# Performance work log

Hardware: AMD Instinct MI355X
Metric: run time of the kernel (lower is better)

The kernel has to match this reference:

```python
import jax, jax.numpy as jnp
import numpy as np
from jax import lax

B, S, P, H = 256, 336, 96, 512


def setup_inputs() -> dict:
    key = jax.random.key(0)
    ks = jax.random.split(key, 18)
    def n(k, shape, s=0.05):
        return jax.random.normal(k, shape, dtype=jnp.float32) * s
    return {
        "x": jax.random.normal(ks[0], (B, S, 7), dtype=jnp.float32),
        "lin_enc_w": n(ks[1], (H, 3)), "lin_enc_b": n(ks[2], (H,)),
        "quat_enc_w": n(ks[3], (H, 4)), "quat_enc_b": n(ks[4], (H,)),
        "lin_wih": n(ks[5], (4 * H, H)), "lin_whh": n(ks[6], (4 * H, H)),
        "lin_bih": n(ks[7], (4 * H,)), "lin_bhh": n(ks[8], (4 * H,)),
        "quat_wih": n(ks[9], (4 * H, H)), "quat_whh": n(ks[10], (4 * H, H)),
        "quat_bih": n(ks[11], (4 * H,)), "quat_bhh": n(ks[12], (4 * H,)),
        "lin_dec_w": n(ks[13], (3, H)), "lin_dec_b": n(ks[14], (3,)),
        "quat_dec_w": n(ks[15], (4, H)), "quat_dec_b": n(ks[16], (4,)),
        "pred_len": P,
    }


def _lstm_cell(carry, xt, Wih, Whh, bih, bhh):
    # PyTorch gate order: i, f, g, o
    h, c = carry
    g = xt @ Wih.T + bih + h @ Whh.T + bhh  # [B, 4H]
    i, f, gg, o = jnp.split(g, 4, axis=-1)
    c = jax.nn.sigmoid(f) * c + jax.nn.sigmoid(i) * jnp.tanh(gg)
    h = jax.nn.sigmoid(o) * jnp.tanh(c)
    return (h, c), h


def _branch(xc, We, be, Wih, Whh, bih, bhh, Wd, bd, pred_len):
    e = xc @ We.T + be  # [B, S, H]
    Bn, _, Hn = e.shape
    cell = lambda carry, xt: _lstm_cell(carry, xt, Wih, Whh, bih, bhh)
    z = jnp.zeros((Bn, Hn), e.dtype)
    (h, _), outs = lax.scan(cell, (z, z), jnp.swapaxes(e, 0, 1))  # outs: [S, B, H]
    # Each prediction step feeds h as input to the LSTM with ZERO initial state
    # (the original code does not pass (h, c) back in).
    def pred_step(h, _):
        (hn, _), _ = cell((jnp.zeros_like(h), jnp.zeros_like(h)), h)
        return hn, hn
    _, preds = lax.scan(pred_step, h, None, length=pred_len)  # [P, B, H]
    seq = jnp.concatenate([outs, preds], axis=0)[1:]  # drop first step -> [S+P-1, B, H]
    return jnp.swapaxes(seq, 0, 1) @ Wd.T + bd


def reference(x, lin_enc_w, lin_enc_b, quat_enc_w, quat_enc_b,
              lin_wih, lin_whh, lin_bih, lin_bhh,
              quat_wih, quat_whh, quat_bih, quat_bhh,
              lin_dec_w, lin_dec_b, quat_dec_w, quat_dec_b, pred_len):
    lx = _branch(x[:, :, :3], lin_enc_w, lin_enc_b, lin_wih, lin_whh,
                 lin_bih, lin_bhh, lin_dec_w, lin_dec_b, pred_len)
    rx = _branch(x[:, :, 3:], quat_enc_w, quat_enc_b, quat_wih, quat_whh,
                 quat_bih, quat_bhh, quat_dec_w, quat_dec_b, pred_len)
    return jnp.concatenate([lx, rx], axis=2)  # [B, S+P-1, 7]
```

## Files before the change

### kernel.cpp

```cpp
#include <hip/hip_runtime.h>

#define BB 256
#define SS 336
#define HH 512
#define NT 431
#define NU 432

typedef __attribute__((ext_vector_type(8))) short bf16x8;
typedef __attribute__((ext_vector_type(16))) float f32x16;
typedef __attribute__((ext_vector_type(4))) int i32x4;


__device__ inline unsigned short f2bf(float f) {
    unsigned int u = __float_as_uint(f);
    unsigned int r = (u + 0x7fffu + ((u >> 16) & 1u)) >> 16;
    return (unsigned short)r;
}
__device__ inline float sigm(float x) { return 1.f / (1.f + __expf(-x)); }
__device__ inline float tanh_(float x) { return 2.f / (1.f + __expf(-2.f * x)) - 1.f; }

__device__ inline i32x4 llc_load_b128(const i32x4* p) {
    i32x4 r;
    asm volatile("global_load_dwordx4 %0, %1, off sc0 sc1" : "=v"(r) : "v"(p));
    return r;
}
__device__ inline void llc_store_b128(i32x4* p, i32x4 v) {
    asm volatile("global_store_dwordx4 %0, %1, off sc0 sc1" :: "v"(p), "v"(v) : "memory");
}
__device__ inline void vm_drain() { asm volatile("s_waitcnt vmcnt(0)" ::: "memory"); }

__global__ void k_wfrag(const float* __restrict__ w0, const float* __restrict__ w1,
                        const float* __restrict__ w2, const float* __restrict__ w3,
                        unsigned short* __restrict__ wfrag) {
    int idx = blockIdx.x * 256 + threadIdx.x;
    int mat = idx >> 17;
    int t = idx & 131071;
    int lane = t & 63;
    int kb = (t >> 6) & 31;
    int wq = (t >> 11) & 3;
    int cg = t >> 13;
    const float* W = mat == 0 ? w0 : (mat == 1 ? w1 : (mat == 2 ? w2 : w3));
    int n = wq * 512 + cg * 32 + (lane & 31);
    int k0 = kb * 16 + (lane >> 5) * 8;
    const float* src = W + n * 512 + k0;
    unsigned short us[8];
#pragma unroll
    for (int j = 0; j < 8; ++j) us[j] = f2bf(src[j]);
    i32x4 v;
    v.x = us[0] | (us[1] << 16); v.y = us[2] | (us[3] << 16);
    v.z = us[4] | (us[5] << 16); v.w = us[6] | (us[7] << 16);
    ((i32x4*)wfrag)[idx] = v;
}

__global__ void k_mbias(const float* __restrict__ lin_wih, const float* __restrict__ quat_wih,
                        const float* __restrict__ lin_enc_w, const float* __restrict__ quat_enc_w,
                        const float* __restrict__ lin_enc_b, const float* __restrict__ quat_enc_b,
                        const float* __restrict__ lin_bih, const float* __restrict__ lin_bhh,
                        const float* __restrict__ quat_bih, const float* __restrict__ quat_bhh,
                        float* __restrict__ M, float* __restrict__ bE, float* __restrict__ bP) {
    int gid = blockIdx.x * 256 + threadIdx.x;
    int branch = gid >> 11;
    int n = gid & 2047;
    int nf = 3 + branch;
    const float* Wih = branch ? quat_wih : lin_wih;
    const float* We  = branch ? quat_enc_w : lin_enc_w;
    const float* be  = branch ? quat_enc_b : lin_enc_b;
    const float* bih = branch ? quat_bih : lin_bih;
    const float* bhh = branch ? quat_bhh : lin_bhh;
    float m[4] = {0.f, 0.f, 0.f, 0.f};
    float bs = 0.f;
    for (int j = 0; j < 512; ++j) {
        float w = Wih[n * 512 + j];
#pragma unroll
        for (int kf = 0; kf < 4; ++kf)
            if (kf < nf) m[kf] += w * We[j * nf + kf];
        bs += w * be[j];
    }
    float* Mp = M + (branch * 2048 + n) * 4;
#pragma unroll
    for (int kf = 0; kf < 4; ++kf) Mp[kf] = m[kf];
    bE[branch * 2048 + n] = bs + bih[n] + bhh[n];
    bP[branch * 2048 + n] = bih[n] + bhh[n];
}

__global__ void k_zero(i32x4* __restrict__ p) {
    int idx = blockIdx.x * 256 + threadIdx.x;
    p[idx] = i32x4{0, 0, 0, 0};
}

__global__ __launch_bounds__(256, 1) void k_persist(
    const float* __restrict__ x,
    const unsigned short* __restrict__ wfrag,
    const float* __restrict__ M, const float* __restrict__ bE, const float* __restrict__ bP,
    const float* __restrict__ lin_dec_w, const float* __restrict__ quat_dec_w,
    const float* __restrict__ lin_dec_b, const float* __restrict__ quat_dec_b,
    unsigned short* __restrict__ hbuf,
    float* __restrict__ out,
    unsigned int* __restrict__ bar) {
    __shared__ i32x4 lds_a[2][2048];
    __shared__ float g_lds[32 * 132];
    __shared__ float h_tile[32 * 33];
    __shared__ float mE[512];
    __shared__ float bEs[128];
    __shared__ float bPs[128];

    const int tid = threadIdx.x;
    const int lane = tid & 63;
    const int wv = tid >> 6;
    const int blk = blockIdx.x;
    const int branch = blk >> 7;
    const int rg = (blk >> 4) & 7;
    const int cg = blk & 15;
    const int group = blk >> 4;
    const int nf = 3 + branch;
    const int row = tid & 31;
    const int jbase = tid >> 5;
    const int b = rg * 32 + row;

    for (int t = tid; t < 512; t += 256) {
        int gate = t >> 7, jj = (t >> 2) & 31, kf = t & 3;
        mE[t] = M[(size_t)(branch * 2048 + gate * 512 + cg * 32 + jj) * 4 + kf];
    }
    if (tid < 128) {
        int gate = tid >> 5, jj = tid & 31;
        bEs[tid] = bE[branch * 2048 + gate * 512 + cg * 32 + jj];
        bPs[tid] = bP[branch * 2048 + gate * 512 + cg * 32 + jj];
    }

    const int dr   = lane & 1;
    const int dd   = (lane >> 1) & 3;
    const int dseg = lane >> 3;
    const int drow = cg * 2 + dr;
    const bool dvalid = dd < nf;
    const float* dwp = (branch ? quat_dec_w : lin_dec_w) + dd * 512;
    const float dbias = dvalid ? (branch ? quat_dec_b : lin_dec_b)[dd] : 0.f;

    const i32x4* BpE = (const i32x4*)wfrag + (size_t)(branch * 2) * 131072
                       + ((cg * 4 + wv) * 32) * 64 + lane;
    const i32x4* BpP = BpE + 131072;
    i32x4 bw[32];
#pragma unroll
    for (int kb = 0; kb < 32; ++kb) bw[kb] = BpE[kb * 64];

    float creg[4] = {0.f, 0.f, 0.f, 0.f};
    unsigned int* myslot = bar + (size_t)blk * 16;

    __syncthreads();

    for (int u = 0; u <= NU; ++u) {
        const int is_enc = (u < SS);

        float xv0 = 0.f, xv1 = 0.f, xv2 = 0.f, xv3 = 0.f;
        if (is_enc) {
            const float* xp = x + ((size_t)b * SS + u) * 7 + branch * 3;
            xv0 = xp[0]; xv1 = xp[1]; xv2 = xp[2];
            if (branch) xv3 = xp[3];
        }
        if (u == SS) {
#pragma unroll
            for (int kb = 0; kb < 32; ++kb) bw[kb] = BpP[kb * 64];
        }

        if (u > 0) {
            if (wv == 0) {
                const unsigned int* slot = bar + (size_t)((group << 4) | (lane & 15)) * 16;
                for (;;) {
                    unsigned int v;
                    asm volatile("global_load_dword %0, %1, off sc0 sc1\n\ts_waitcnt vmcnt(0)"
                                 : "=v"(v) : "v"(slot) : "memory");
                    if (__all((int)(v >= (unsigned int)u))) break;
                    __builtin_amdgcn_s_sleep(1);
                }
            }
            __syncthreads();
        }

        i32x4* lds_cur = lds_a[u & 1];
        {
            const i32x4* gsrc = (const i32x4*)hbuf + (size_t)(u & 1) * 32768
                                + (size_t)branch * 16384 + rg * 2048 + tid;
            i32x4 av[8];
#pragma unroll
            for (int i = 0; i < 8; ++i) av[i] = llc_load_b128(gsrc + i * 256);
            vm_drain();
            __builtin_amdgcn_sched_barrier(0);
#pragma unroll
            for (int i = 0; i < 8; ++i) lds_cur[i * 256 + tid] = av[i];
        }
        __syncthreads();

        if (u == NU) {
            if (wv == 3) {
                float s = 0.f;
                if (dvalid) {
                    const unsigned short* hp = (const unsigned short*)lds_cur;
#pragma unroll
                    for (int jj = 0; jj < 64; ++jj) {
                        int j = dseg * 64 + jj;
                        unsigned short hu = hp[(j >> 4) * 512 + ((j >> 3) & 1) * 256 + drow * 8 + (j & 7)];
                        s += __uint_as_float(((unsigned int)hu) << 16) * dwp[j];
                    }
                }
                s += __shfl_xor(s, 8);
                s += __shfl_xor(s, 16);
                s += __shfl_xor(s, 32);
                if (dseg == 0 && dvalid)
                    out[((size_t)(rg * 32 + drow) * NT + (u - 2)) * 7 + branch * 3 + dd] = s + dbias;
            }
            break;
        }

        f32x16 acc = {};
        const i32x4* Afrag = lds_cur + lane;
#pragma unroll
        for (int kb = 0; kb < 32; ++kb) {
            i32x4 a0 = Afrag[kb * 64];
            acc = __builtin_amdgcn_mfma_f32_32x32x16_bf16(*(const bf16x8*)&a0, *(const bf16x8*)&bw[kb], acc, 0, 0, 0);
        }
        {
            int col_l = wv * 32 + (lane & 31);
            int rbase = 4 * (lane >> 5);
#pragma unroll
            for (int r = 0; r < 16; ++r) {
                int row_l = rbase + (r & 3) + 8 * (r >> 2);
                g_lds[row_l * 132 + col_l] = acc[r];
            }
        }
        __syncthreads();

#pragma unroll
        for (int p = 0; p < 4; ++p) {
            int jj = jbase * 4 + p;
            float gi = g_lds[row * 132 + jj];
            float gf = g_lds[row * 132 + 32 + jj];
            float gc = g_lds[row * 132 + 64 + jj];
            float go = g_lds[row * 132 + 96 + jj];
            if (is_enc) {
                int j4 = jj * 4;
                gi += bEs[jj]      + xv0 * mE[j4]       + xv1 * mE[j4 + 1]       + xv2 * mE[j4 + 2]       + xv3 * mE[j4 + 3];
                gf += bEs[32 + jj] + xv0 * mE[128 + j4] + xv1 * mE[128 + j4 + 1] + xv2 * mE[128 + j4 + 2] + xv3 * mE[128 + j4 + 3];
                gc += bEs[64 + jj] + xv0 * mE[256 + j4] + xv1 * mE[256 + j4 + 1] + xv2 * mE[256 + j4 + 2] + xv3 * mE[256 + j4 + 3];
                go += bEs[96 + jj] + xv0 * mE[384 + j4] + xv1 * mE[384 + j4 + 1] + xv2 * mE[384 + j4 + 2] + xv3 * mE[384 + j4 + 3];
            } else {
                gi += bPs[jj];
                gf += bPs[32 + jj];
                gc += bPs[64 + jj];
                go += bPs[96 + jj];
            }
            float iv = sigm(gi), fv = sigm(gf), gv = tanh_(gc), ov = sigm(go);
            float cn;
            if (is_enc) {
                cn = fv * creg[p] + iv * gv;
                creg[p] = cn;
            } else {
                cn = iv * gv;
            }
            h_tile[row * 33 + jj] = ov * tanh_(cn);
        }
        __syncthreads();

        if (wv == 0) {
#pragma unroll
            for (int chunk = 0; chunk < 2; ++chunk) {
                int row_l = lane & 31;
                int ch = chunk * 16 + (lane >> 5) * 8;
                unsigned short us[8];
#pragma unroll
                for (int j = 0; j < 8; ++j) us[j] = f2bf(h_tile[row_l * 33 + ch + j]);
                i32x4 v;
                v.x = us[0] | (us[1] << 16); v.y = us[2] | (us[3] << 16);
                v.z = us[4] | (us[5] << 16); v.w = us[6] | (us[7] << 16);
                int kb = cg * 2 + chunk;
                llc_store_b128((i32x4*)hbuf + (size_t)((u + 1) & 1) * 32768
                               + (size_t)branch * 16384 + rg * 2048 + kb * 64 + lane, v);
            }
            vm_drain();
            if (lane == 0) {
                unsigned int fl = (unsigned int)(u + 1);
                asm volatile("global_store_dword %0, %1, off sc0 sc1" :: "v"(myslot), "v"(fl) : "memory");
            }
        } else if (wv == 3 && u >= 2) {
            float s = 0.f;
            if (dvalid) {
                const unsigned short* hp = (const unsigned short*)lds_cur;
#pragma unroll
                for (int jj = 0; jj < 64; ++jj) {
                    int j = dseg * 64 + jj;
                    unsigned short hu = hp[(j >> 4) * 512 + ((j >> 3) & 1) * 256 + drow * 8 + (j & 7)];
                    s += __uint_as_float(((unsigned int)hu) << 16) * dwp[j];
                }
            }
            s += __shfl_xor(s, 8);
            s += __shfl_xor(s, 16);
            s += __shfl_xor(s, 32);
            if (dseg == 0 && dvalid)
                out[((size_t)(rg * 32 + drow) * NT + (u - 2)) * 7 + branch * 3 + dd] = s + dbias;
        }
    }
}

extern "C" void kernel_launch(void* const* d_in, const int* in_sizes, int n_in,
                              void* d_out, int out_size, void* d_ws, size_t ws_size,
                              hipStream_t stream) {
    const float* x          = (const float*)d_in[0];
    const float* lin_enc_w  = (const float*)d_in[1];
    const float* lin_enc_b  = (const float*)d_in[2];
    const float* quat_enc_w = (const float*)d_in[3];
    const float* quat_enc_b = (const float*)d_in[4];
    const float* lin_wih    = (const float*)d_in[5];
    const float* lin_whh    = (const float*)d_in[6];
    const float* lin_bih    = (const float*)d_in[7];
    const float* lin_bhh    = (const float*)d_in[8];
    const float* quat_wih   = (const float*)d_in[9];
    const float* quat_whh   = (const float*)d_in[10];
    const float* quat_bih   = (const float*)d_in[11];
    const float* quat_bhh   = (const float*)d_in[12];
    const float* lin_dec_w  = (const float*)d_in[13];
    const float* lin_dec_b  = (const float*)d_in[14];
    const float* quat_dec_w = (const float*)d_in[15];
    const float* quat_dec_b = (const float*)d_in[16];
    float* out = (float*)d_out;
    char* ws = (char*)d_ws;

    unsigned short* wfrag = (unsigned short*)(ws + 0);
    unsigned short* hbuf  = (unsigned short*)(ws + 8388608ull);
    unsigned int*   bar   = (unsigned int*)(ws + 9437184ull);
    float* M    = (float*)(ws + 10485760ull);
    float* bE   = (float*)(ws + 10551296ull);
    float* bP   = (float*)(ws + 10567680ull);

    k_wfrag<<<2048, 256, 0, stream>>>(lin_whh, lin_wih, quat_whh, quat_wih, wfrag);
    k_mbias<<<16, 256, 0, stream>>>(lin_wih, quat_wih, lin_enc_w, quat_enc_w,
                                    lin_enc_b, quat_enc_b, lin_bih, lin_bhh,
                                    quat_bih, quat_bhh, M, bE, bP);
    k_zero<<<260, 256, 0, stream>>>((i32x4*)(ws + 8388608ull));

    k_persist<<<256, 256, 0, stream>>>(x, wfrag, M, bE, bP, lin_dec_w, quat_dec_w,
                                       lin_dec_b, quat_dec_b, hbuf, out, bar);
}
```

Measured before the change: 2.997 ms.

## Interleave two batch cohorts per persistent block to hide inter-block barrier latency

```diff
diff --git a/kernel.cpp b/kernel.cpp
--- a/kernel.cpp
+++ b/kernel.cpp
@@ -98,7 +98,7 @@
     float* __restrict__ out,
     unsigned int* __restrict__ bar) {
     __shared__ i32x4 lds_a[2][2048];
-    __shared__ float g_lds[32 * 132];
+    __shared__ float g_lds[32 * 133];
     __shared__ float h_tile[32 * 33];
     __shared__ float mE[512];
     __shared__ float bEs[128];
@@ -108,15 +108,12 @@
     const int lane = tid & 63;
     const int wv = tid >> 6;
     const int blk = blockIdx.x;
-    const int branch = blk >> 7;
-    const int rg = (blk >> 4) & 7;
+    const int branch = blk >> 6;
+    const int rgl = (blk >> 4) & 3;
     const int cg = blk & 15;
-    const int group = blk >> 4;
     const int nf = 3 + branch;
     const int row = tid & 31;
     const int jbase = tid >> 5;
-    const int b = rg * 32 + row;
-
     for (int t = tid; t < 512; t += 256) {
         int gate = t >> 7, jj = (t >> 2) & 31, kf = t & 3;
         mE[t] = M[(size_t)(branch * 2048 + gate * 512 + cg * 32 + jj) * 4 + kf];
@@ -142,55 +139,154 @@
 #pragma unroll
     for (int kb = 0; kb < 32; ++kb) bw[kb] = BpE[kb * 64];
 
-    float creg[4] = {0.f, 0.f, 0.f, 0.f};
-    unsigned int* myslot = bar + (size_t)blk * 16;
+    float creg[2][4] = {{0.f, 0.f, 0.f, 0.f}, {0.f, 0.f, 0.f, 0.f}};
 
     __syncthreads();
 
     for (int u = 0; u <= NU; ++u) {
         const int is_enc = (u < SS);
-
-        float xv0 = 0.f, xv1 = 0.f, xv2 = 0.f, xv3 = 0.f;
-        if (is_enc) {
-            const float* xp = x + ((size_t)b * SS + u) * 7 + branch * 3;
-            xv0 = xp[0]; xv1 = xp[1]; xv2 = xp[2];
-            if (branch) xv3 = xp[3];
-        }
         if (u == SS) {
 #pragma unroll
             for (int kb = 0; kb < 32; ++kb) bw[kb] = BpP[kb * 64];
         }
 
-        if (u > 0) {
+#pragma unroll
+        for (int coh = 0; coh < 2; ++coh) {
+            const int rgt = coh * 4 + rgl;
+            const int b = coh * 128 + rgl * 32 + row;
+
+            float xv0 = 0.f, xv1 = 0.f, xv2 = 0.f, xv3 = 0.f;
+            if (is_enc) {
+                const float* xp = x + ((size_t)b * SS + u) * 7 + branch * 3;
+                xv0 = xp[0]; xv1 = xp[1]; xv2 = xp[2];
+                if (branch) xv3 = xp[3];
+            }
+
+            if (u > 0) {
+                if (wv == 0) {
+                    const unsigned int* slot = bar
+                        + (size_t)((((branch << 3) | (coh << 2) | rgl) << 4) | (lane & 15)) * 16;
+                    int guard = 0;
+                    for (;;) {
+                        unsigned int v = 0xFFFFFFFFu;
+                        if (lane < 16)
+                            asm volatile("global_load_dword %0, %1, off sc0 sc1\n\ts_waitcnt vmcnt(0)"
+                                         : "=v"(v) : "v"(slot) : "memory");
+                        if (__all((int)(v >= (unsigned int)u))) break;
+                        if (++guard > (1 << 18)) break;
+                        __builtin_amdgcn_s_sleep(1);
+                    }
+                }
+                __syncthreads();
+            }
+
+            i32x4* lds_cur = lds_a[coh];
+            {
+                const i32x4* gsrc = (const i32x4*)hbuf + (size_t)(u & 1) * 32768
+                                    + (size_t)branch * 16384 + rgt * 2048 + tid;
+                i32x4 av[8];
+#pragma unroll
+                for (int i = 0; i < 8; ++i) av[i] = llc_load_b128(gsrc + i * 256);
+                vm_drain();
+                __builtin_amdgcn_sched_barrier(0);
+#pragma unroll
+                for (int i = 0; i < 8; ++i) lds_cur[i * 256 + tid] = av[i];
+            }
+            __syncthreads();
+
+            if (u == NU) {
+                if (wv == 3) {
+                    float s = 0.f;
+                    if (dvalid) {
+                        const unsigned short* hp = (const unsigned short*)lds_cur;
+#pragma unroll
+                        for (int jj = 0; jj < 64; ++jj) {
+                            int j = dseg * 64 + jj;
+                            unsigned short hu = hp[(j >> 4) * 512 + ((j >> 3) & 1) * 256 + drow * 8 + (j & 7)];
+                            s += __uint_as_float(((unsigned int)hu) << 16) * dwp[j];
+                        }
+                    }
+                    s += __shfl_xor(s, 8);
+                    s += __shfl_xor(s, 16);
+                    s += __shfl_xor(s, 32);
+                    if (dseg == 0 && dvalid)
+                        out[((size_t)(coh * 128 + rgl * 32 + drow) * NT + (u - 2)) * 7 + branch * 3 + dd] = s + dbias;
+                }
+                continue;
+            }
+
+            f32x16 acc = {};
+            const i32x4* Afrag = lds_cur + lane;
+#pragma unroll
+            for (int kb = 0; kb < 32; ++kb) {
+                i32x4 a0 = Afrag[kb * 64];
+                acc = __builtin_amdgcn_mfma_f32_32x32x16_bf16(*(const bf16x8*)&a0, *(const bf16x8*)&bw[kb], acc, 0, 0, 0);
+            }
+            {
+                int col_l = wv * 32 + (lane & 31);
+                int rbase = 4 * (lane >> 5);
+#pragma unroll
+                for (int r = 0; r < 16; ++r) {
+                    int row_l = rbase + (r & 3) + 8 * (r >> 2);
+                    g_lds[row_l * 133 + col_l] = acc[r];
+                }
+            }
+            __syncthreads();
+
+#pragma unroll
+            for (int p = 0; p < 4; ++p) {
+                int jj = jbase * 4 + p;
+                float gi = g_lds[row * 133 + jj];
+                float gf = g_lds[row * 133 + 32 + jj];
+                float gc = g_lds[row * 133 + 64 + jj];
+                float go = g_lds[row * 133 + 96 + jj];
+                if (is_enc) {
+                    int j4 = jj * 4;
+                    gi += bEs[jj]      + xv0 * mE[j4]       + xv1 * mE[j4 + 1]       + xv2 * mE[j4 + 2]       + xv3 * mE[j4 + 3];
+                    gf += bEs[32 + jj] + xv0 * mE[128 + j4] + xv1 * mE[128 + j4 + 1] + xv2 * mE[128 + j4 + 2] + xv3 * mE[128 + j4 + 3];
+                    gc += bEs[64 + jj] + xv0 * mE[256 + j4] + xv1 * mE[256 + j4 + 1] + xv2 * mE[256 + j4 + 2] + xv3 * mE[256 + j4 + 3];
+                    go += bEs[96 + jj] + xv0 * mE[384 + j4] + xv1 * mE[384 + j4 + 1] + xv2 * mE[384 + j4 + 2] + xv3 * mE[384 + j4 + 3];
+                } else {
+                    gi += bPs[jj];
+                    gf += bPs[32 + jj];
+                    gc += bPs[64 + jj];
+                    go += bPs[96 + jj];
+                }
+                float iv = sigm(gi), fv = sigm(gf), gv = tanh_(gc), ov = sigm(go);
+                float cn;
+                if (is_enc) {
+                    cn = fv * creg[coh][p] + iv * gv;
+                    creg[coh][p] = cn;
+                } else {
+                    cn = iv * gv;
+                }
+                h_tile[row * 33 + jj] = ov * tanh_(cn);
+            }
+            __syncthreads();
+
             if (wv == 0) {
-                const unsigned int* slot = bar + (size_t)((group << 4) | (lane & 15)) * 16;
-                for (;;) {
-                    unsigned int v;
-                    asm volatile("global_load_dword %0, %1, off sc0 sc1\n\ts_waitcnt vmcnt(0)"
-                                 : "=v"(v) : "v"(slot) : "memory");
-                    if (__all((int)(v >= (unsigned int)u))) break;
-                    __builtin_amdgcn_s_sleep(1);
-                }
-            }
-            __syncthreads();
-        }
-
-        i32x4* lds_cur = lds_a[u & 1];
-        {
-            const i32x4* gsrc = (const i32x4*)hbuf + (size_t)(u & 1) * 32768
-                                + (size_t)branch * 16384 + rg * 2048 + tid;
-            i32x4 av[8];
-#pragma unroll
-            for (int i = 0; i < 8; ++i) av[i] = llc_load_b128(gsrc + i * 256);
-            vm_drain();
-            __builtin_amdgcn_sched_barrier(0);
-#pragma unroll
-            for (int i = 0; i < 8; ++i) lds_cur[i * 256 + tid] = av[i];
-        }
-        __syncthreads();
-
-        if (u == NU) {
-            if (wv == 3) {
+#pragma unroll
+                for (int chunk = 0; chunk < 2; ++chunk) {
+                    int row_l = lane & 31;
+                    int ch = chunk * 16 + (lane >> 5) * 8;
+                    unsigned short us[8];
+#pragma unroll
+                    for (int j = 0; j < 8; ++j) us[j] = f2bf(h_tile[row_l * 33 + ch + j]);
+                    i32x4 v;
+                    v.x = us[0] | (us[1] << 16); v.y = us[2] | (us[3] << 16);
+                    v.z = us[4] | (us[5] << 16); v.w = us[6] | (us[7] << 16);
+                    int kb = cg * 2 + chunk;
+                    llc_store_b128((i32x4*)hbuf + (size_t)((u + 1) & 1) * 32768
+                                   + (size_t)branch * 16384 + rgt * 2048 + kb * 64 + lane, v);
+                }
+                vm_drain();
+                if (lane == 0) {
+                    unsigned int fl = (unsigned int)(u + 1);
+                    unsigned int* myslot = bar
+                        + (size_t)((((branch << 3) | (coh << 2) | rgl) << 4) | cg) * 16;
+                    asm volatile("global_store_dword %0, %1, off sc0 sc1" :: "v"(myslot), "v"(fl) : "memory");
+                }
+            } else if (wv == 3 && u >= 2) {
                 float s = 0.f;
                 if (dvalid) {
                     const unsigned short* hp = (const unsigned short*)lds_cur;
@@ -205,97 +301,11 @@
                 s += __shfl_xor(s, 16);
                 s += __shfl_xor(s, 32);
                 if (dseg == 0 && dvalid)
-                    out[((size_t)(rg * 32 + drow) * NT + (u - 2)) * 7 + branch * 3 + dd] = s + dbias;
-            }
-            break;
+                    out[((size_t)(coh * 128 + rgl * 32 + drow) * NT + (u - 2)) * 7 + branch * 3 + dd] = s + dbias;
+            }
         }
 
-        f32x16 acc = {};
-        const i32x4* Afrag = lds_cur + lane;
-#pragma unroll
-        for (int kb = 0; kb < 32; ++kb) {
-            i32x4 a0 = Afrag[kb * 64];
-            acc = __builtin_amdgcn_mfma_f32_32x32x16_bf16(*(const bf16x8*)&a0, *(const bf16x8*)&bw[kb], acc, 0, 0, 0);
-        }
-        {
-            int col_l = wv * 32 + (lane & 31);
-            int rbase = 4 * (lane >> 5);
-#pragma unroll
-            for (int r = 0; r < 16; ++r) {
-                int row_l = rbase + (r & 3) + 8 * (r >> 2);
-                g_lds[row_l * 132 + col_l] = acc[r];
-            }
-        }
-        __syncthreads();
-
-#pragma unroll
-        for (int p = 0; p < 4; ++p) {
-            int jj = jbase * 4 + p;
-            float gi = g_lds[row * 132 + jj];
-            float gf = g_lds[row * 132 + 32 + jj];
-            float gc = g_lds[row * 132 + 64 + jj];
-            float go = g_lds[row * 132 + 96 + jj];
-            if (is_enc) {
-                int j4 = jj * 4;
-                gi += bEs[jj]      + xv0 * mE[j4]       + xv1 * mE[j4 + 1]       + xv2 * mE[j4 + 2]       + xv3 * mE[j4 + 3];
-                gf += bEs[32 + jj] + xv0 * mE[128 + j4] + xv1 * mE[128 + j4 + 1] + xv2 * mE[128 + j4 + 2] + xv3 * mE[128 + j4 + 3];
-                gc += bEs[64 + jj] + xv0 * mE[256 + j4] + xv1 * mE[256 + j4 + 1] + xv2 * mE[256 + j4 + 2] + xv3 * mE[256 + j4 + 3];
-                go += bEs[96 + jj] + xv0 * mE[384 + j4] + xv1 * mE[384 + j4 + 1] + xv2 * mE[384 + j4 + 2] + xv3 * mE[384 + j4 + 3];
-            } else {
-                gi += bPs[jj];
-                gf += bPs[32 + jj];
-                gc += bPs[64 + jj];
-                go += bPs[96 + jj];
-            }
-            float iv = sigm(gi), fv = sigm(gf), gv = tanh_(gc), ov = sigm(go);
-            float cn;
-            if (is_enc) {
-                cn = fv * creg[p] + iv * gv;
-                creg[p] = cn;
-            } else {
-                cn = iv * gv;
-            }
-            h_tile[row * 33 + jj] = ov * tanh_(cn);
-        }
-        __syncthreads();
-
-        if (wv == 0) {
-#pragma unroll
-            for (int chunk = 0; chunk < 2; ++chunk) {
-                int row_l = lane & 31;
-                int ch = chunk * 16 + (lane >> 5) * 8;
-                unsigned short us[8];
-#pragma unroll
-                for (int j = 0; j < 8; ++j) us[j] = f2bf(h_tile[row_l * 33 + ch + j]);
-                i32x4 v;
-                v.x = us[0] | (us[1] << 16); v.y = us[2] | (us[3] << 16);
-                v.z = us[4] | (us[5] << 16); v.w = us[6] | (us[7] << 16);
-                int kb = cg * 2 + chunk;
-                llc_store_b128((i32x4*)hbuf + (size_t)((u + 1) & 1) * 32768
-                               + (size_t)branch * 16384 + rg * 2048 + kb * 64 + lane, v);
-            }
-            vm_drain();
-            if (lane == 0) {
-                unsigned int fl = (unsigned int)(u + 1);
-                asm volatile("global_store_dword %0, %1, off sc0 sc1" :: "v"(myslot), "v"(fl) : "memory");
-            }
-        } else if (wv == 3 && u >= 2) {
-            float s = 0.f;
-            if (dvalid) {
-                const unsigned short* hp = (const unsigned short*)lds_cur;
-#pragma unroll
-                for (int jj = 0; jj < 64; ++jj) {
-                    int j = dseg * 64 + jj;
-                    unsigned short hu = hp[(j >> 4) * 512 + ((j >> 3) & 1) * 256 + drow * 8 + (j & 7)];
-                    s += __uint_as_float(((unsigned int)hu) << 16) * dwp[j];
-                }
-            }
-            s += __shfl_xor(s, 8);
-            s += __shfl_xor(s, 16);
-            s += __shfl_xor(s, 32);
-            if (dseg == 0 && dvalid)
-                out[((size_t)(rg * 32 + drow) * NT + (u - 2)) * 7 + branch * 3 + dd] = s + dbias;
-        }
+        if (u == NU) break;
     }
 }
 
@@ -335,6 +345,6 @@
                                     quat_bih, quat_bhh, M, bE, bP);
     k_zero<<<260, 256, 0, stream>>>((i32x4*)(ws + 8388608ull));
 
-    k_persist<<<256, 256, 0, stream>>>(x, wfrag, M, bE, bP, lin_dec_w, quat_dec_w,
+    k_persist<<<128, 256, 0, stream>>>(x, wfrag, M, bE, bP, lin_dec_w, quat_dec_w,
                                        lin_dec_b, quat_dec_b, hbuf, out, bar);
 }
```

New measurement: 4.954 ms. 1.65x slower.
